# Kernel tuning notes

Measured on AMD Instinct MI355X. Metric: run time of the kernel, lower is better.

The kernel has to match this reference:

```python
import jax, jax.numpy as jnp
import numpy as np

B, T = 64, 2048
RNN_DIM, EMB_DIM, ATTN_DIM = 1024, 512, 128
N_FILT, KSIZE = 32, 31
PAD = (KSIZE - 1) // 2


def setup_inputs() -> dict:
    key = jax.random.key(0)
    ks = jax.random.split(key, 8)
    s = 0.02
    return {
        "attention_hidden_state": jax.random.normal(ks[0], (B, RNN_DIM), jnp.float32),
        "memory": jax.random.normal(ks[1], (B, T, EMB_DIM), jnp.float32),
        "processed_memory": jax.random.normal(ks[2], (B, T, ATTN_DIM), jnp.float32),
        "attention_weights_cat": jax.random.uniform(ks[3], (B, 2, T), jnp.float32),
        "mask": jnp.zeros((B, T), dtype=bool),
        "Wq": jax.random.normal(ks[4], (ATTN_DIM, RNN_DIM), jnp.float32) * s,
        "Wconv": jax.random.normal(ks[5], (N_FILT, 2, KSIZE), jnp.float32) * s,
        "Wloc": jax.random.normal(ks[6], (ATTN_DIM, N_FILT), jnp.float32) * s,
        "Wv": jax.random.normal(ks[7], (1, ATTN_DIM), jnp.float32) * s,
    }


def reference(attention_hidden_state, memory, processed_memory,
              attention_weights_cat, mask, Wq, Wconv, Wloc, Wv):
    # query projection: [B, rnn] -> [B, 1, attn]
    pq = jnp.einsum("br,ar->ba", attention_hidden_state, Wq)[:, None, :]
    # location conv: [B, 2, T] -> [B, F, T]
    conv = jax.lax.conv_general_dilated(
        attention_weights_cat, Wconv, window_strides=(1,),
        padding=[(PAD, PAD)], dimension_numbers=("NCH", "OIH", "NCH"))
    # [B, T, F] @ Wloc.T -> [B, T, attn]
    ploc = jnp.einsum("bft,af->bta", conv, Wloc)
    # energies: [B, T]
    energies = jnp.einsum("bta,oa->bto", jnp.tanh(pq + ploc + processed_memory), Wv)[..., 0]
    alignment = jnp.where(mask, -jnp.inf, energies)
    attention_weights = jax.nn.softmax(alignment, axis=1)
    # context: [B, emb]
    attention_context = jnp.einsum("bt,bte->be", attention_weights, memory)
    return attention_context, attention_weights
```

## Files before the change

kernel.cpp:

```cpp
#include <hip/hip_runtime.h>
#include <math.h>

#define BB 64
#define TT 2048
#define RNN 1024
#define EMB 512
#define ATTN 128
#define NF 32
#define KS 31
#define PADW 15

#define TILE_T 256
#define NSEG 16
#define SEG_T (TT / NSEG)

__global__ __launch_bounds__(256) void pq_kernel(const float* __restrict__ h,
                                                 const float* __restrict__ Wq,
                                                 float* __restrict__ pq) {
    int b = blockIdx.x;
    __shared__ float s_h[RNN];
    for (int i = threadIdx.x; i < RNN; i += 256) s_h[i] = h[b * RNN + i];
    __syncthreads();

    int wave = threadIdx.x >> 6;
    int lane = threadIdx.x & 63;
    for (int j = 0; j < 32; ++j) {
        int a = wave * 32 + j;
        const float4* wq4 = (const float4*)(Wq + (size_t)a * RNN);
        float acc = 0.f;
#pragma unroll
        for (int i = 0; i < 4; ++i) {
            float4 w4 = wq4[lane + 64 * i];
            float4 h4 = *(const float4*)(s_h + 4 * (lane + 64 * i));
            acc += w4.x * h4.x + w4.y * h4.y + w4.z * h4.z + w4.w * h4.w;
        }
#pragma unroll
        for (int off = 32; off > 0; off >>= 1) acc += __shfl_xor(acc, off, 64);
        if (lane == 0) pq[b * ATTN + a] = acc;
    }
}

__global__ __launch_bounds__(256) void energy_kernel(
    const float* __restrict__ pm,
    const float* __restrict__ awc,
    const float* __restrict__ pq,
    const float* __restrict__ Wconv,
    const float* __restrict__ Wloc,
    const float* __restrict__ Wv,
    float* __restrict__ energies)
{
    int b = blockIdx.x >> 3;
    int t0 = (blockIdx.x & 7) * TILE_T;
    int tid = threadIdx.x;

    __shared__ float s_awc[2][TILE_T + 2 * PADW];
    __shared__ float s_conv[TILE_T][36];

    for (int i = tid; i < 2 * (TILE_T + 2 * PADW); i += 256) {
        int c = i / (TILE_T + 2 * PADW);
        int j = i % (TILE_T + 2 * PADW);
        int tg = t0 - PADW + j;
        s_awc[c][j] = (tg >= 0 && tg < TT) ? awc[((size_t)b * 2 + c) * TT + tg] : 0.f;
    }
    __syncthreads();

    float aw[2][KS];
#pragma unroll
    for (int c = 0; c < 2; ++c)
#pragma unroll
        for (int k = 0; k < KS; ++k) aw[c][k] = s_awc[c][tid + k];

#pragma unroll
    for (int f = 0; f < NF; ++f) {
        float acc = 0.f;
#pragma unroll
        for (int c = 0; c < 2; ++c)
#pragma unroll
            for (int k = 0; k < KS; ++k)
                acc += aw[c][k] * Wconv[(f * 2 + c) * KS + k];
        s_conv[tid][f] = acc;
    }
    __syncthreads();

    int wave = tid >> 6;
    int lane = tid & 63;

    float wl0[NF], wl1[NF];
#pragma unroll
    for (int f = 0; f < NF; ++f) {
        wl0[f] = Wloc[lane * NF + f];
        wl1[f] = Wloc[(lane + 64) * NF + f];
    }
    float pq0 = pq[b * ATTN + lane], pq1 = pq[b * ATTN + lane + 64];
    float wv0 = Wv[lane], wv1 = Wv[lane + 64];

    for (int i = 0; i < 64; ++i) {
        int tl = wave * 64 + i;
        int tg = t0 + tl;
        float v0 = pq0, v1 = pq1;
        const float4* cv4 = (const float4*)&s_conv[tl][0];
#pragma unroll
        for (int f4 = 0; f4 < 8; ++f4) {
            float4 cv = cv4[f4];
            v0 += cv.x * wl0[f4 * 4 + 0] + cv.y * wl0[f4 * 4 + 1] +
                  cv.z * wl0[f4 * 4 + 2] + cv.w * wl0[f4 * 4 + 3];
            v1 += cv.x * wl1[f4 * 4 + 0] + cv.y * wl1[f4 * 4 + 1] +
                  cv.z * wl1[f4 * 4 + 2] + cv.w * wl1[f4 * 4 + 3];
        }
        const float* pmrow = pm + ((size_t)(b * TT + tg)) * ATTN;
        v0 += pmrow[lane];
        v1 += pmrow[lane + 64];
        float e = wv0 * tanhf(v0) + wv1 * tanhf(v1);
#pragma unroll
        for (int off = 32; off > 0; off >>= 1) e += __shfl_xor(e, off, 64);
        if (lane == 0) energies[b * TT + tg] = e;
    }
}

__global__ __launch_bounds__(256) void softmax_kernel(
    const float* __restrict__ energies, const unsigned char* __restrict__ mask,
    float* __restrict__ w) {
    int b = blockIdx.x, tid = threadIdx.x;
    __shared__ float s_red[8];

    float v[8];
    float m = -1e30f;
#pragma unroll
    for (int i = 0; i < 8; ++i) {
        int t = i * 256 + tid;
        float e = energies[b * TT + t];
        if (mask[(size_t)b * TT + t] != 0) e = -1e30f;
        v[i] = e;
        m = fmaxf(m, e);
    }
#pragma unroll
    for (int off = 32; off > 0; off >>= 1) m = fmaxf(m, __shfl_xor(m, off, 64));
    int wave = tid >> 6, lane = tid & 63;
    if (lane == 0) s_red[wave] = m;
    __syncthreads();
    m = fmaxf(fmaxf(s_red[0], s_red[1]), fmaxf(s_red[2], s_red[3]));

    float ssum = 0.f;
#pragma unroll
    for (int i = 0; i < 8; ++i) {
        v[i] = expf(v[i] - m);
        ssum += v[i];
    }
#pragma unroll
    for (int off = 32; off > 0; off >>= 1) ssum += __shfl_xor(ssum, off, 64);
    if (lane == 0) s_red[4 + wave] = ssum;
    __syncthreads();
    float inv = 1.f / (s_red[4] + s_red[5] + s_red[6] + s_red[7]);
#pragma unroll
    for (int i = 0; i < 8; ++i) w[b * TT + i * 256 + tid] = v[i] * inv;
}

__global__ __launch_bounds__(256) void ctx_partial_kernel(
    const float* __restrict__ mem,
    const float* __restrict__ w,
    float* __restrict__ partial)
{
    int b = blockIdx.x >> 4;
    int seg = blockIdx.x & 15;
    int tid = threadIdx.x;

    __shared__ float s_w[SEG_T];
    if (tid < SEG_T) s_w[tid] = w[b * TT + seg * SEG_T + tid];
    __syncthreads();

    float2 acc = {0.f, 0.f};
    const float2* m2 =
        (const float2*)(mem + ((size_t)b * TT + (size_t)seg * SEG_T) * EMB) + tid;
#pragma unroll 4
    for (int i = 0; i < SEG_T; ++i) {
        float wv = s_w[i];
        float2 mv = m2[(size_t)i * (EMB / 2)];
        acc.x += wv * mv.x;
        acc.y += wv * mv.y;
    }
    float2* p2 = (float2*)(partial + ((size_t)(seg * BB + b)) * EMB) + tid;
    *p2 = acc;
}

__global__ __launch_bounds__(256) void ctx_reduce_kernel(
    const float* __restrict__ partial, float* __restrict__ ctx) {
    int idx = blockIdx.x * 256 + threadIdx.x;
    float acc = 0.f;
#pragma unroll
    for (int s = 0; s < NSEG; ++s) acc += partial[(size_t)s * (BB * EMB) + idx];
    ctx[idx] = acc;
}

extern "C" void kernel_launch(void* const* d_in, const int* in_sizes, int n_in,
                              void* d_out, int out_size, void* d_ws, size_t ws_size,
                              hipStream_t stream) {
    const float* h    = (const float*)d_in[0];
    const float* mem  = (const float*)d_in[1];
    const float* pmem = (const float*)d_in[2];
    const float* awc  = (const float*)d_in[3];
    const unsigned char* mask = (const unsigned char*)d_in[4];
    const float* Wq   = (const float*)d_in[5];
    const float* Wcv  = (const float*)d_in[6];
    const float* Wloc = (const float*)d_in[7];
    const float* Wv   = (const float*)d_in[8];

    float* out = (float*)d_out;
    float* ctx = out;
    float* wts = out + BB * EMB;

    float* ws       = (float*)d_ws;
    float* pq       = ws;
    float* energies = ws + BB * ATTN;
    float* partial  = ws + BB * ATTN + BB * TT;

    pq_kernel<<<BB, 256, 0, stream>>>(h, Wq, pq);
    energy_kernel<<<BB * (TT / TILE_T), 256, 0, stream>>>(pmem, awc, pq, Wcv,
                                                          Wloc, Wv, energies);
    softmax_kernel<<<BB, 256, 0, stream>>>(energies, mask, wts);
    ctx_partial_kernel<<<BB * NSEG, 256, 0, stream>>>(mem, wts, partial);
    ctx_reduce_kernel<<<(BB * EMB) / 256, 256, 0, stream>>>(partial, ctx);
}
```

Measured before the change: 156.7 us.

## Halve energy tile, split conv filters, fast tanh/exp, float4 context partials

Shrinks the energy tile to 128 timesteps, which doubles the block count, and splits the 32 conv filters across two thread halves. It replaces tanhf with an exp/reciprocal-based fast tanh and expf with __expf, and collects each wave's energies into lanes so they are written in one coalesced store. The context partial kernel now uses float4 loads with two thread halves covering alternating timesteps, which doubles the number of partials the reduce kernel must sum. The fast math gives up a little accuracy, and the extra partials add reduce traffic.

Measured after the change: 143.8 us. 8.3% less time.

```diff
diff --git a/kernel.cpp b/kernel.cpp
--- a/kernel.cpp
+++ b/kernel.cpp
@@ -10,9 +10,17 @@
 #define KS 31
 #define PADW 15
 
-#define TILE_T 256
+#define TILE_T 128
 #define NSEG 16
 #define SEG_T (TT / NSEG)
+#define NPART (NSEG * 2)
+
+__device__ __forceinline__ float fast_tanh(float x) {
+    float ax = fabsf(x);
+    float e = __expf(-2.f * ax);
+    float r = (1.f - e) * __builtin_amdgcn_rcpf(1.f + e);
+    return copysignf(r, x);
+}
 
 __global__ __launch_bounds__(256) void pq_kernel(const float* __restrict__ h,
                                                  const float* __restrict__ Wq,
@@ -49,8 +57,8 @@
     const float* __restrict__ Wv,
     float* __restrict__ energies)
 {
-    int b = blockIdx.x >> 3;
-    int t0 = (blockIdx.x & 7) * TILE_T;
+    int b = blockIdx.x >> 4;
+    int t0 = (blockIdx.x & 15) * TILE_T;
     int tid = threadIdx.x;
 
     __shared__ float s_awc[2][TILE_T + 2 * PADW];
@@ -64,21 +72,26 @@
     }
     __syncthreads();
 
-    float aw[2][KS];
-#pragma unroll
-    for (int c = 0; c < 2; ++c)
-#pragma unroll
-        for (int k = 0; k < KS; ++k) aw[c][k] = s_awc[c][tid + k];
-
-#pragma unroll
-    for (int f = 0; f < NF; ++f) {
-        float acc = 0.f;
+    {
+        int t = tid & 127;
+        int fh = tid >> 7;
+        float aw[2][KS];
 #pragma unroll
         for (int c = 0; c < 2; ++c)
 #pragma unroll
-            for (int k = 0; k < KS; ++k)
-                acc += aw[c][k] * Wconv[(f * 2 + c) * KS + k];
-        s_conv[tid][f] = acc;
+            for (int k = 0; k < KS; ++k) aw[c][k] = s_awc[c][t + k];
+
+#pragma unroll
+        for (int ff = 0; ff < 16; ++ff) {
+            int f = fh * 16 + ff;
+            float acc = 0.f;
+#pragma unroll
+            for (int c = 0; c < 2; ++c)
+#pragma unroll
+                for (int k = 0; k < KS; ++k)
+                    acc += aw[c][k] * Wconv[(f * 2 + c) * KS + k];
+            s_conv[t][f] = acc;
+        }
     }
     __syncthreads();
 
@@ -94,8 +107,10 @@
     float pq0 = pq[b * ATTN + lane], pq1 = pq[b * ATTN + lane + 64];
     float wv0 = Wv[lane], wv1 = Wv[lane + 64];
 
-    for (int i = 0; i < 64; ++i) {
-        int tl = wave * 64 + i;
+    float eout = 0.f;
+#pragma unroll 2
+    for (int i = 0; i < 32; ++i) {
+        int tl = wave * 32 + i;
         int tg = t0 + tl;
         float v0 = pq0, v1 = pq1;
         const float4* cv4 = (const float4*)&s_conv[tl][0];
@@ -110,11 +125,12 @@
         const float* pmrow = pm + ((size_t)(b * TT + tg)) * ATTN;
         v0 += pmrow[lane];
         v1 += pmrow[lane + 64];
-        float e = wv0 * tanhf(v0) + wv1 * tanhf(v1);
+        float e = wv0 * fast_tanh(v0) + wv1 * fast_tanh(v1);
 #pragma unroll
         for (int off = 32; off > 0; off >>= 1) e += __shfl_xor(e, off, 64);
-        if (lane == 0) energies[b * TT + tg] = e;
-    }
+        if (lane == i) eout = e;
+    }
+    if (lane < 32) energies[b * TT + t0 + wave * 32 + lane] = eout;
 }
 
 __global__ __launch_bounds__(256) void softmax_kernel(
@@ -143,7 +159,7 @@
     float ssum = 0.f;
 #pragma unroll
     for (int i = 0; i < 8; ++i) {
-        v[i] = expf(v[i] - m);
+        v[i] = __expf(v[i] - m);
         ssum += v[i];
     }
 #pragma unroll
@@ -163,23 +179,27 @@
     int b = blockIdx.x >> 4;
     int seg = blockIdx.x & 15;
     int tid = threadIdx.x;
+    int e4 = tid & 127;
+    int half = tid >> 7;
 
     __shared__ float s_w[SEG_T];
     if (tid < SEG_T) s_w[tid] = w[b * TT + seg * SEG_T + tid];
     __syncthreads();
 
-    float2 acc = {0.f, 0.f};
-    const float2* m2 =
-        (const float2*)(mem + ((size_t)b * TT + (size_t)seg * SEG_T) * EMB) + tid;
+    float4 acc = {0.f, 0.f, 0.f, 0.f};
+    const float4* m4 = (const float4*)(mem + ((size_t)b * TT + (size_t)seg * SEG_T) * EMB)
+                       + (size_t)half * (EMB / 4) + e4;
 #pragma unroll 4
-    for (int i = 0; i < SEG_T; ++i) {
-        float wv = s_w[i];
-        float2 mv = m2[(size_t)i * (EMB / 2)];
+    for (int i = 0; i < SEG_T / 2; ++i) {
+        float wv = s_w[2 * i + half];
+        float4 mv = m4[(size_t)i * (2 * EMB / 4)];
         acc.x += wv * mv.x;
         acc.y += wv * mv.y;
-    }
-    float2* p2 = (float2*)(partial + ((size_t)(seg * BB + b)) * EMB) + tid;
-    *p2 = acc;
+        acc.z += wv * mv.z;
+        acc.w += wv * mv.w;
+    }
+    float4* p4 = (float4*)(partial + ((size_t)(seg * 2 + half) * BB + b) * EMB) + e4;
+    *p4 = acc;
 }
 
 __global__ __launch_bounds__(256) void ctx_reduce_kernel(
@@ -187,7 +207,7 @@
     int idx = blockIdx.x * 256 + threadIdx.x;
     float acc = 0.f;
 #pragma unroll
-    for (int s = 0; s < NSEG; ++s) acc += partial[(size_t)s * (BB * EMB) + idx];
+    for (int s = 0; s < NPART; ++s) acc += partial[(size_t)s * (BB * EMB) + idx];
     ctx[idx] = acc;
 }
 
```
